# Kernel optimization log

Hardware: AMD Instinct MI355X
Metric: run time of the kernel (lower is better)

## Reference

```python
import jax, jax.numpy as jnp
import numpy as np

FS = 30.0   # sampling_rate from __init__
B, T = 32768, 2048


def setup_inputs() -> dict:
    key = jax.random.key(0)
    x = jax.random.normal(key, (B, T), dtype=jnp.float32)
    return {"x": x}


def _trapz_slice(pairs, a, b):
    # trapz of s[a:b] with dx=1/FS, given precomputed trapezoid pairs
    # pairs[i] = 0.5*(s[i]+s[i+1]); integral sums i in [a, b-2]. Empty slice -> 0.
    i = jnp.arange(pairs.shape[0])
    m = ((i >= a) & (i <= b - 2)).astype(pairs.dtype)
    return jnp.sum(pairs * m) / FS


def _features(s):
    n = s.shape[0]
    # ---- time-domain: [max, ptp, var(ddof=1), std(ddof=1)] ----
    mx = jnp.max(s)
    ptp = mx - jnp.min(s)
    var = jnp.var(s, ddof=1)
    std = jnp.sqrt(var)
    # ---- frequency-domain: mean |FFT| ----
    mean_amp = jnp.mean(jnp.abs(jnp.fft.fft(s)))
    # ---- peak / valley detection on interior points (index i+1 in signal) ----
    l, m_, r = s[:-2], s[1:-1], s[2:]
    peak_m = (l < m_) & (m_ > r)
    val_m = (l > m_) & (m_ < r)
    n_peaks = jnp.sum(peak_m)
    n_vals = jnp.sum(val_m)
    pos = jnp.arange(n - 2)
    p0 = jnp.argmax(peak_m) + 1                       # peaks[0]
    v0 = jnp.argmax(val_m) + 1                        # valleys[0]
    v1 = jnp.argmax(val_m & (pos > (v0 - 1))) + 1     # valleys[1]
    vlast = (n - 3) - jnp.argmax(val_m[::-1]) + 1     # valleys[-1]
    # ---- iPPG features ----
    pairs = 0.5 * (s[:-1] + s[1:])
    PA = _trapz_slice(pairs, v0, vlast)
    A2 = _trapz_slice(pairs, p0, v1)
    PH = s[p0] - s[v0]
    A1 = _trapz_slice(pairs, v0, p0)
    # half-height width between valleys[0] and peaks[0]
    half = 0.5 * (s[p0] + s[v0])
    idx = jnp.arange(n)
    lm = (idx >= v0) & (idx < p0) & (s >= half)
    left_i = jnp.where(jnp.any(lm), jnp.argmax(lm), v0)
    rm = (idx <= p0) & (idx > v0) & (s >= half)
    right_i = jnp.where(jnp.any(rm), (n - 1) - jnp.argmax(rm[::-1]), p0)
    PWHH = (right_i - left_i).astype(s.dtype) / FS
    ippg = jnp.stack([PA, A2, PH, A1, PWHH])
    ippg = jnp.where((n_peaks >= 1) & (n_vals >= 2), ippg, jnp.zeros(5, s.dtype))
    return jnp.concatenate([jnp.stack([mx, ptp, var, std, mean_amp]), ippg])


def reference(x):
    return jax.vmap(_features)(x)  # [B, 10]
```

## Files before the change

kernel.cpp:

```cpp
#include <hip/hip_runtime.h>
#include <math.h>

#define NTH 256

#define CMUL(vr, vi, c, s) { float _tr = (vr)*(c) - (vi)*(s); (vi) = (vr)*(s) + (vi)*(c); (vr) = _tr; }

#define FFT4(r0,i0,r1,i1,r2,i2,r3,i3) {                     \
    float _acr=(r0)+(r2), _aci=(i0)+(i2);                   \
    float _scr=(r0)-(r2), _sci=(i0)-(i2);                   \
    float _bdr=(r1)+(r3), _bdi=(i1)+(i3);                   \
    float _sdr=(r1)-(r3), _sdi=(i1)-(i3);                   \
    (r0)=_acr+_bdr; (i0)=_aci+_bdi;                         \
    (r1)=_scr+_sdi; (i1)=_sci-_sdr;                         \
    (r2)=_acr-_bdr; (i2)=_aci-_bdi;                         \
    (r3)=_scr-_sdi; (i3)=_sci+_sdr; }

__device__ __forceinline__ void fft16(float* xr, float* xi) {
    const float C1 = 0.92387953251128675613f;
    const float S1 = 0.38268343236508977172f;
    const float R2 = 0.70710678118654752440f;
#pragma unroll
    for (int q = 0; q < 4; ++q)
        FFT4(xr[q], xi[q], xr[4+q], xi[4+q], xr[8+q], xi[8+q], xr[12+q], xi[12+q]);
    CMUL(xr[5],  xi[5],   C1, -S1);
    CMUL(xr[9],  xi[9],   R2, -R2);
    CMUL(xr[13], xi[13],  S1, -C1);
    CMUL(xr[6],  xi[6],   R2, -R2);
    { float t = xr[10]; xr[10] = xi[10]; xi[10] = -t; }
    CMUL(xr[14], xi[14], -R2, -R2);
    CMUL(xr[7],  xi[7],   S1, -C1);
    CMUL(xr[11], xi[11], -R2, -R2);
    CMUL(xr[15], xi[15], -C1,  S1);
#pragma unroll
    for (int s = 0; s < 4; ++s)
        FFT4(xr[4*s], xi[4*s], xr[4*s+1], xi[4*s+1], xr[4*s+2], xi[4*s+2], xr[4*s+3], xi[4*s+3]);
}

__global__ __launch_bounds__(NTH, 2)
void feat_kernel(const float* __restrict__ gx, float* __restrict__ gout) {
    const int tid = threadIdx.x;
    const int wv  = tid >> 6;
    const int ln  = tid & 63;
    const int row = blockIdx.x * 4 + wv;
    const float* xrow = gx + (size_t)row * 2048;
    float* orow = gout + (size_t)row * 10;

    __shared__ float ZRs[4][1024], ZIs[4][1024];
    float* Zr = ZRs[wv];
    float* Zi = ZIs[wv];

    const int al  = ln & 3;
    const int k2r = ln >> 2;
    const int b5  = ln >> 5;

    const float4* x4 = (const float4*)xrow;
#pragma unroll
    for (int t = 0; t < 8; ++t) {
        float4 u = x4[ln + 64 * t];
        int c  = 2 * ln + 128 * t;
        int a0 = c ^ (2 * t + b5);
        int a1 = a0 ^ 1;
        Zr[a0] = u.x; Zi[a0] = u.y;
        Zr[a1] = u.z; Zi[a1] = u.w;
    }

    float r[32];
    {
        int base = 16 * ln;
#pragma unroll
        for (int j = 0; j < 16; ++j) {
            int a = base + (j ^ k2r);
            r[2*j]   = Zr[a];
            r[2*j+1] = Zi[a];
        }
    }

    float vmax = r[0], vmin = r[0], vsum = 0.0f, vsq = 0.0f;
#pragma unroll
    for (int e = 0; e < 32; ++e) {
        vmax = fmaxf(vmax, r[e]); vmin = fminf(vmin, r[e]);
        vsum += r[e]; vsq = fmaf(r[e], r[e], vsq);
    }
#pragma unroll
    for (int o = 1; o < 64; o <<= 1) {
        vmax = fmaxf(vmax, __shfl_xor(vmax, o, 64));
        vmin = fminf(vmin, __shfl_xor(vmin, o, 64));
        vsum += __shfl_xor(vsum, o, 64);
        vsq  += __shfl_xor(vsq,  o, 64);
    }
    {
        float mean = vsum * (1.0f / 2048.0f);
        float var = (vsq - vsum * mean) * (1.0f / 2047.0f);
        if (ln == 0) {
            orow[0] = vmax;
            orow[1] = vmax - vmin;
            orow[2] = var;
            orow[3] = sqrtf(var);
        }
    }

    float lN = __shfl_up(r[31], 1, 64);
    unsigned aw = 0, bw = 0;
#pragma unroll
    for (int m = 0; m < 32; ++m) {
        float l = (m == 0) ? lN : r[m - 1];
        float c = r[m];
        aw |= (unsigned)(l < c) << m;
        bw |= (unsigned)(l > c) << m;
    }
    unsigned an = __shfl_down(aw, 1, 64) & 1u;
    unsigned bn = __shfl_down(bw, 1, 64) & 1u;
    unsigned pm = aw & ((bw >> 1) | (bn << 31));
    unsigned vm = bw & ((aw >> 1) | (an << 31));
    if (ln == 0)  { pm &= ~1u; vm &= ~1u; }
    if (ln == 63) { pm &= 0x7FFFFFFFu; vm &= 0x7FFFFFFFu; }

    int pk = __popc(pm) | (__popc(vm) << 12);
    int mp = pm ? 32 * ln + __ffs(pm) - 1 : (1 << 30);
    int mv = vm ? 32 * ln + __ffs(vm) - 1 : (1 << 30);
    int Mv = vm ? 32 * ln + 31 - __clz(vm) : -1;
#pragma unroll
    for (int o = 1; o < 64; o <<= 1) {
        pk += __shfl_xor(pk, o, 64);
        mp = min(mp, __shfl_xor(mp, o, 64));
        mv = min(mv, __shfl_xor(mv, o, 64));
        Mv = max(Mv, __shfl_xor(Mv, o, 64));
    }
    const int n_peaks = pk & 0xFFF, n_vals = pk >> 12, p0 = mp, v0 = mv, vlast = Mv;

    {
        float PA = 0.0f, A2f = 0.0f, PH = 0.0f, A1f = 0.0f, PW = 0.0f;
        if (n_peaks >= 1 && n_vals >= 2) {
            int lo = v0 - 32 * ln;
            unsigned sel = (lo < 0) ? 0xFFFFFFFFu : ((lo >= 31) ? 0u : (0xFFFFFFFFu << (lo + 1)));
            unsigned m2 = vm & sel;
            int mv2 = m2 ? 32 * ln + __ffs(m2) - 1 : (1 << 30);
#pragma unroll
            for (int o = 1; o < 64; o <<= 1) mv2 = min(mv2, __shfl_xor(mv2, o, 64));
            const int v1 = mv2;

            auto sAt = [&](int p) -> float {
                int e = p >> 1;
                int a = e ^ (e >> 6);
                return (p & 1) ? Zi[a] : Zr[a];
            };
            float s_v0  = sAt(v0), s_p0 = sAt(p0);
            float s_pm1 = sAt(p0 - 1), s_v1m1 = sAt(v1 - 1), s_vLm1 = sAt(vlast - 1);
            PH = s_p0 - s_v0;
            float half = 0.5f * (s_p0 + s_v0);

            float S1 = 0.0f, S2 = 0.0f, S3 = 0.0f;
            int li = 1 << 30, ri = -1;
#pragma unroll
            for (int m = 0; m < 32; ++m) {
                int i = 32 * ln + m;
                float si = r[m];
                bool geV0 = (i >= v0), geP0 = (i >= p0);
                if (geV0 && !geP0)  S1 += si;
                if (geP0 && i < v1) S2 += si;
                if (geV0 && i < vlast) S3 += si;
                if (si >= half) {
                    if (geV0 && !geP0)     li = min(li, i);
                    if (i > v0 && i <= p0) ri = max(ri, i);
                }
            }
#pragma unroll
            for (int o = 1; o < 64; o <<= 1) {
                S1 += __shfl_xor(S1, o, 64);
                S2 += __shfl_xor(S2, o, 64);
                S3 += __shfl_xor(S3, o, 64);
                li = min(li, __shfl_xor(li, o, 64));
                ri = max(ri, __shfl_xor(ri, o, 64));
            }
            PA  = (S3 - 0.5f * (s_v0 + s_vLm1)) * (1.0f / 30.0f);
            A2f = (v1 > p0) ? (S2 - 0.5f * (s_p0 + s_v1m1)) * (1.0f / 30.0f) : 0.0f;
            A1f = (p0 > v0) ? (S1 - 0.5f * (s_v0 + s_pm1)) * (1.0f / 30.0f) : 0.0f;
            if (li == (1 << 30)) li = v0;
            if (ri < 0)          ri = p0;
            PW = (float)(ri - li) * (1.0f / 30.0f);
        }
        if (ln == 0) {
            orow[5] = PA;
            orow[6] = A2f;
            orow[7] = PH;
            orow[8] = A1f;
            orow[9] = PW;
        }
    }

    float s0, c0;
    __sincosf((float)ln * (-3.14159265358979323846f / 1024.0f), &s0, &c0);

    float ar[16], ai[16];
#pragma unroll
    for (int n2 = 0; n2 < 16; ++n2) {
        int a = (ln ^ n2) + 64 * n2;
        ar[n2] = Zr[a];
        ai[n2] = Zi[a];
    }
    fft16(ar, ai);
    {
        const float cb = c0 * c0 - s0 * s0;
        const float sb = 2.0f * c0 * s0;
        int wb = 16 * ln;
        Zr[wb + k2r] = ar[0];
        Zi[wb + k2r] = ai[0];
        float cc = cb, ss = sb;
#pragma unroll
        for (int k2 = 1; k2 < 16; ++k2) {
            const int idx = (k2 >> 2) + 4 * (k2 & 3);
            CMUL(ar[idx], ai[idx], cc, ss);
            int a = wb + (k2 ^ k2r);
            Zr[a] = ar[idx];
            Zi[a] = ai[idx];
            float nc = cc * cb - ss * sb;
            ss = cc * sb + ss * cb;
            cc = nc;
        }
    }
    {
        int cbase = 16 * al;
#pragma unroll
        for (int b = 0; b < 16; ++b) {
            int a = cbase + (k2r ^ b) + 64 * b;
            ar[b] = Zr[a];
            ai[b] = Zi[a];
        }
    }
    fft16(ar, ai);
    {
        float cA = (al & 1) ? 0.99518472667219688624f : 1.0f;
        float sA = (al & 1) ? -0.09801714032956060199f : 0.0f;
        float cB = (al & 1) ? 0.95694033573220886494f : 0.98078528040323044913f;
        float sB = (al & 1) ? -0.29028467725446236764f : -0.19509032201612826785f;
        float c1 = (al & 2) ? cB : cA;
        float s1 = (al & 2) ? sB : sA;
        float cc = c1, ss = s1;
#pragma unroll
        for (int j = 1; j < 16; ++j) {
            const int idx = (j >> 2) + 4 * (j & 3);
            CMUL(ar[idx], ai[idx], cc, ss);
            float nc = cc * c1 - ss * s1;
            ss = cc * s1 + ss * c1;
            cc = nc;
        }
    }
    {
        const bool hi = (al & 2) != 0;
        const bool b0 = (al & 1) != 0;
        const int g = ((al & 1) << 1) | (al >> 1);
        int fbase = k2r + 256 * g;
#pragma unroll
        for (int idx = 0; idx < 16; ++idx) {
            int j = (idx >> 2) + 4 * (idx & 3);
            float tr = __shfl_xor(ar[idx], 2, 64);
            float ti = __shfl_xor(ai[idx], 2, 64);
            float vr = hi ? (tr - ar[idx]) : (ar[idx] + tr);
            float vi = hi ? (ti - ai[idx]) : (ai[idx] + ti);
            float sr = __shfl_xor(vr, 1, 64);
            float si = __shfl_xor(vi, 1, 64);
            float Xr, Xi;
            if (!b0) { Xr = hi ? (vr + si) : (vr + sr); Xi = hi ? (vi - sr) : (vi + si); }
            else     { Xr = hi ? (sr - vi) : (sr - vr); Xi = hi ? (si + vr) : (si - vi); }
            Zr[fbase + 16 * j] = Xr;
            Zi[fbase + 16 * j] = Xi;
        }
    }

    float amp = 0.0f;
    {
        float rc = c0, rs = s0;
        const float C16 = 0.98078528040323044913f, S16 = 0.19509032201612826785f;
#pragma unroll
        for (int t = 0; t < 8; ++t) {
            int k = ln + 64 * t;
            int m = (1024 - k) & 1023;
            float zr = Zr[k], zi = Zi[k];
            float mr = Zr[m], mi = Zi[m];
            float Er = 0.5f * (zr + mr), Ei = 0.5f * (zi - mi);
            float Or = 0.5f * (zi + mi), Oi = 0.5f * (mr - zr);
            float Pr = Or * rc - Oi * rs, Pi = Or * rs + Oi * rc;
            float x1r = Er + Pr, x1i = Ei + Pi;
            float x2r = Er - Pr, x2i = Ei - Pi;
            amp += 2.0f * (__builtin_amdgcn_sqrtf(x1r * x1r + x1i * x1i) +
                           __builtin_amdgcn_sqrtf(x2r * x2r + x2i * x2i));
            float nr = rc * C16 + rs * S16;
            rs = rs * C16 - rc * S16;
            rc = nr;
        }
        {
            float zr0 = Zr[0], zi0 = Zi[0];
            float q1 = zr0 + zi0, q2 = zr0 - zi0;
            float corr0 = __builtin_amdgcn_sqrtf(q1 * q1) + __builtin_amdgcn_sqrtf(q2 * q2);
            float zr5 = Zr[512], zi5 = Zi[512];
            float c512 = 2.0f * __builtin_amdgcn_sqrtf(zr5 * zr5 + zi5 * zi5);
            amp += (ln == 0) ? (c512 - corr0) : 0.0f;
        }
    }
#pragma unroll
    for (int o = 1; o < 64; o <<= 1) amp += __shfl_xor(amp, o, 64);

    if (ln == 0) {
        orow[4] = amp * (1.0f / 2048.0f);
    }
}

extern "C" void kernel_launch(void* const* d_in, const int* in_sizes, int n_in,
                              void* d_out, int out_size, void* d_ws, size_t ws_size,
                              hipStream_t stream) {
    (void)d_ws; (void)ws_size; (void)n_in; (void)out_size;
    const float* x = (const float*)d_in[0];
    float* out = (float*)d_out;
    int rows = in_sizes[0] / 2048;
    feat_kernel<<<dim3(rows / 4), dim3(NTH), 0, stream>>>(x, out);
}
```

Measured before the change: 394.9 us.

## Interleave real/imag in shared memory and vectorize FFT math with float2

Replaces the split real/imaginary shared arrays with an interleaved float2 array, so each complex load or store becomes a single 64-bit LDS access instead of two 32-bit ones. The FFT butterflies, twiddle multiplies, statistics and the real-FFT postprocessing are rewritten with 2-wide vector types, which lets the compiler emit packed FP32 instructions. The cost is a possible change in LDS bank-conflict behaviour with 8-byte accesses under the existing XOR swizzles, and possibly more register pressure.

```diff
diff --git a/kernel.cpp b/kernel.cpp
--- a/kernel.cpp
+++ b/kernel.cpp
@@ -3,37 +3,39 @@
 
 #define NTH 256
 
-#define CMUL(vr, vi, c, s) { float _tr = (vr)*(c) - (vi)*(s); (vi) = (vr)*(s) + (vi)*(c); (vr) = _tr; }
-
-#define FFT4(r0,i0,r1,i1,r2,i2,r3,i3) {                     \
-    float _acr=(r0)+(r2), _aci=(i0)+(i2);                   \
-    float _scr=(r0)-(r2), _sci=(i0)-(i2);                   \
-    float _bdr=(r1)+(r3), _bdi=(i1)+(i3);                   \
-    float _sdr=(r1)-(r3), _sdi=(i1)-(i3);                   \
-    (r0)=_acr+_bdr; (i0)=_aci+_bdi;                         \
-    (r1)=_scr+_sdi; (i1)=_sci-_sdr;                         \
-    (r2)=_acr-_bdr; (i2)=_aci-_bdi;                         \
-    (r3)=_scr-_sdi; (i3)=_sci+_sdr; }
-
-__device__ __forceinline__ void fft16(float* xr, float* xi) {
+typedef __attribute__((ext_vector_type(2))) float v2f;
+
+__device__ __forceinline__ v2f cmulv(v2f z, float c, float s) {
+    v2f t; t.x = -z.y; t.y = z.x;
+    return z * c + t * s;
+}
+
+#define FFT4V(z0,z1,z2,z3) {                      \
+    v2f _ac = (z0) + (z2), _sc = (z0) - (z2);     \
+    v2f _bd = (z1) + (z3), _sd = (z1) - (z3);     \
+    v2f _jd; _jd.x = _sd.y; _jd.y = -_sd.x;       \
+    (z0) = _ac + _bd;                             \
+    (z1) = _sc + _jd;                             \
+    (z2) = _ac - _bd;                             \
+    (z3) = _sc - _jd; }
+
+__device__ __forceinline__ void fft16v(v2f* z) {
     const float C1 = 0.92387953251128675613f;
     const float S1 = 0.38268343236508977172f;
     const float R2 = 0.70710678118654752440f;
 #pragma unroll
-    for (int q = 0; q < 4; ++q)
-        FFT4(xr[q], xi[q], xr[4+q], xi[4+q], xr[8+q], xi[8+q], xr[12+q], xi[12+q]);
-    CMUL(xr[5],  xi[5],   C1, -S1);
-    CMUL(xr[9],  xi[9],   R2, -R2);
-    CMUL(xr[13], xi[13],  S1, -C1);
-    CMUL(xr[6],  xi[6],   R2, -R2);
-    { float t = xr[10]; xr[10] = xi[10]; xi[10] = -t; }
-    CMUL(xr[14], xi[14], -R2, -R2);
-    CMUL(xr[7],  xi[7],   S1, -C1);
-    CMUL(xr[11], xi[11], -R2, -R2);
-    CMUL(xr[15], xi[15], -C1,  S1);
-#pragma unroll
-    for (int s = 0; s < 4; ++s)
-        FFT4(xr[4*s], xi[4*s], xr[4*s+1], xi[4*s+1], xr[4*s+2], xi[4*s+2], xr[4*s+3], xi[4*s+3]);
+    for (int q = 0; q < 4; ++q) FFT4V(z[q], z[4+q], z[8+q], z[12+q]);
+    z[5]  = cmulv(z[5],   C1, -S1);
+    z[9]  = cmulv(z[9],   R2, -R2);
+    z[13] = cmulv(z[13],  S1, -C1);
+    z[6]  = cmulv(z[6],   R2, -R2);
+    { v2f t; t.x = z[10].y; t.y = -z[10].x; z[10] = t; }
+    z[14] = cmulv(z[14], -R2, -R2);
+    z[7]  = cmulv(z[7],   S1, -C1);
+    z[11] = cmulv(z[11], -R2, -R2);
+    z[15] = cmulv(z[15], -C1,  S1);
+#pragma unroll
+    for (int s = 0; s < 4; ++s) FFT4V(z[4*s], z[4*s+1], z[4*s+2], z[4*s+3]);
 }
 
 __global__ __launch_bounds__(NTH, 2)
@@ -45,9 +47,8 @@
     const float* xrow = gx + (size_t)row * 2048;
     float* orow = gout + (size_t)row * 10;
 
-    __shared__ float ZRs[4][1024], ZIs[4][1024];
-    float* Zr = ZRs[wv];
-    float* Zi = ZIs[wv];
+    __shared__ v2f Zs_[4][1024];
+    v2f* Zs = Zs_[wv];
 
     const int al  = ln & 3;
     const int k2r = ln >> 2;
@@ -60,27 +61,31 @@
         int c  = 2 * ln + 128 * t;
         int a0 = c ^ (2 * t + b5);
         int a1 = a0 ^ 1;
-        Zr[a0] = u.x; Zi[a0] = u.y;
-        Zr[a1] = u.z; Zi[a1] = u.w;
-    }
-
-    float r[32];
+        v2f w0; w0.x = u.x; w0.y = u.y;
+        v2f w1; w1.x = u.z; w1.y = u.w;
+        Zs[a0] = w0;
+        Zs[a1] = w1;
+    }
+
+    v2f r2[16];
     {
         int base = 16 * ln;
 #pragma unroll
-        for (int j = 0; j < 16; ++j) {
-            int a = base + (j ^ k2r);
-            r[2*j]   = Zr[a];
-            r[2*j+1] = Zi[a];
-        }
-    }
-
-    float vmax = r[0], vmin = r[0], vsum = 0.0f, vsq = 0.0f;
-#pragma unroll
-    for (int e = 0; e < 32; ++e) {
-        vmax = fmaxf(vmax, r[e]); vmin = fminf(vmin, r[e]);
-        vsum += r[e]; vsq = fmaf(r[e], r[e], vsq);
-    }
+        for (int j = 0; j < 16; ++j)
+            r2[j] = Zs[base + (j ^ k2r)];
+    }
+
+    v2f mx2 = r2[0], mn2 = r2[0], sm2 = r2[0], sq2 = r2[0] * r2[0];
+#pragma unroll
+    for (int j = 1; j < 16; ++j) {
+        v2f e = r2[j];
+        mx2.x = fmaxf(mx2.x, e.x); mx2.y = fmaxf(mx2.y, e.y);
+        mn2.x = fminf(mn2.x, e.x); mn2.y = fminf(mn2.y, e.y);
+        sm2 += e;
+        sq2 = e * e + sq2;
+    }
+    float vmax = fmaxf(mx2.x, mx2.y), vmin = fminf(mn2.x, mn2.y);
+    float vsum = sm2.x + sm2.y, vsq = sq2.x + sq2.y;
 #pragma unroll
     for (int o = 1; o < 64; o <<= 1) {
         vmax = fmaxf(vmax, __shfl_xor(vmax, o, 64));
@@ -99,14 +104,16 @@
         }
     }
 
-    float lN = __shfl_up(r[31], 1, 64);
+    float lN = __shfl_up(r2[15].y, 1, 64);
     unsigned aw = 0, bw = 0;
 #pragma unroll
-    for (int m = 0; m < 32; ++m) {
-        float l = (m == 0) ? lN : r[m - 1];
-        float c = r[m];
-        aw |= (unsigned)(l < c) << m;
-        bw |= (unsigned)(l > c) << m;
+    for (int j = 0; j < 16; ++j) {
+        float pv = (j == 0) ? lN : r2[j - 1].y;
+        float e0 = r2[j].x, e1 = r2[j].y;
+        aw |= (unsigned)(pv < e0) << (2 * j);
+        bw |= (unsigned)(pv > e0) << (2 * j);
+        aw |= (unsigned)(e0 < e1) << (2 * j + 1);
+        bw |= (unsigned)(e0 > e1) << (2 * j + 1);
     }
     unsigned an = __shfl_down(aw, 1, 64) & 1u;
     unsigned bn = __shfl_down(bw, 1, 64) & 1u;
@@ -141,8 +148,8 @@
 
             auto sAt = [&](int p) -> float {
                 int e = p >> 1;
-                int a = e ^ (e >> 6);
-                return (p & 1) ? Zi[a] : Zr[a];
+                v2f zz = Zs[e ^ (e >> 6)];
+                return (p & 1) ? zz.y : zz.x;
             };
             float s_v0  = sAt(v0), s_p0 = sAt(p0);
             float s_pm1 = sAt(p0 - 1), s_v1m1 = sAt(v1 - 1), s_vLm1 = sAt(vlast - 1);
@@ -152,16 +159,19 @@
             float S1 = 0.0f, S2 = 0.0f, S3 = 0.0f;
             int li = 1 << 30, ri = -1;
 #pragma unroll
-            for (int m = 0; m < 32; ++m) {
-                int i = 32 * ln + m;
-                float si = r[m];
-                bool geV0 = (i >= v0), geP0 = (i >= p0);
-                if (geV0 && !geP0)  S1 += si;
-                if (geP0 && i < v1) S2 += si;
-                if (geV0 && i < vlast) S3 += si;
-                if (si >= half) {
-                    if (geV0 && !geP0)     li = min(li, i);
-                    if (i > v0 && i <= p0) ri = max(ri, i);
+            for (int j = 0; j < 16; ++j) {
+#pragma unroll
+                for (int h = 0; h < 2; ++h) {
+                    int i = 32 * ln + 2 * j + h;
+                    float si = h ? r2[j].y : r2[j].x;
+                    bool geV0 = (i >= v0), geP0 = (i >= p0);
+                    if (geV0 && !geP0)  S1 += si;
+                    if (geP0 && i < v1) S2 += si;
+                    if (geV0 && i < vlast) S3 += si;
+                    if (si >= half) {
+                        if (geV0 && !geP0)     li = min(li, i);
+                        if (i > v0 && i <= p0) ri = max(ri, i);
+                    }
                 }
             }
 #pragma unroll
@@ -191,43 +201,32 @@
     float s0, c0;
     __sincosf((float)ln * (-3.14159265358979323846f / 1024.0f), &s0, &c0);
 
-    float ar[16], ai[16];
-#pragma unroll
-    for (int n2 = 0; n2 < 16; ++n2) {
-        int a = (ln ^ n2) + 64 * n2;
-        ar[n2] = Zr[a];
-        ai[n2] = Zi[a];
-    }
-    fft16(ar, ai);
+    v2f az[16];
+#pragma unroll
+    for (int n2 = 0; n2 < 16; ++n2)
+        az[n2] = Zs[(ln ^ n2) + 64 * n2];
+    fft16v(az);
     {
         const float cb = c0 * c0 - s0 * s0;
         const float sb = 2.0f * c0 * s0;
         int wb = 16 * ln;
-        Zr[wb + k2r] = ar[0];
-        Zi[wb + k2r] = ai[0];
-        float cc = cb, ss = sb;
+        Zs[wb + k2r] = az[0];
+        v2f w; w.x = cb; w.y = sb;
 #pragma unroll
         for (int k2 = 1; k2 < 16; ++k2) {
             const int idx = (k2 >> 2) + 4 * (k2 & 3);
-            CMUL(ar[idx], ai[idx], cc, ss);
-            int a = wb + (k2 ^ k2r);
-            Zr[a] = ar[idx];
-            Zi[a] = ai[idx];
-            float nc = cc * cb - ss * sb;
-            ss = cc * sb + ss * cb;
-            cc = nc;
+            az[idx] = cmulv(az[idx], w.x, w.y);
+            Zs[wb + (k2 ^ k2r)] = az[idx];
+            w = cmulv(w, cb, sb);
         }
     }
     {
         int cbase = 16 * al;
 #pragma unroll
-        for (int b = 0; b < 16; ++b) {
-            int a = cbase + (k2r ^ b) + 64 * b;
-            ar[b] = Zr[a];
-            ai[b] = Zi[a];
-        }
-    }
-    fft16(ar, ai);
+        for (int b = 0; b < 16; ++b)
+            az[b] = Zs[cbase + (k2r ^ b) + 64 * b];
+    }
+    fft16v(az);
     {
         float cA = (al & 1) ? 0.99518472667219688624f : 1.0f;
         float sA = (al & 1) ? -0.09801714032956060199f : 0.0f;
@@ -235,14 +234,12 @@
         float sB = (al & 1) ? -0.29028467725446236764f : -0.19509032201612826785f;
         float c1 = (al & 2) ? cB : cA;
         float s1 = (al & 2) ? sB : sA;
-        float cc = c1, ss = s1;
+        v2f w; w.x = c1; w.y = s1;
 #pragma unroll
         for (int j = 1; j < 16; ++j) {
             const int idx = (j >> 2) + 4 * (j & 3);
-            CMUL(ar[idx], ai[idx], cc, ss);
-            float nc = cc * c1 - ss * s1;
-            ss = cc * s1 + ss * c1;
-            cc = nc;
+            az[idx] = cmulv(az[idx], w.x, w.y);
+            w = cmulv(w, c1, s1);
         }
     }
     {
@@ -253,47 +250,48 @@
 #pragma unroll
         for (int idx = 0; idx < 16; ++idx) {
             int j = (idx >> 2) + 4 * (idx & 3);
-            float tr = __shfl_xor(ar[idx], 2, 64);
-            float ti = __shfl_xor(ai[idx], 2, 64);
-            float vr = hi ? (tr - ar[idx]) : (ar[idx] + tr);
-            float vi = hi ? (ti - ai[idx]) : (ai[idx] + ti);
+            float arx = az[idx].x, aix = az[idx].y;
+            float tr = __shfl_xor(arx, 2, 64);
+            float ti = __shfl_xor(aix, 2, 64);
+            float vr = hi ? (tr - arx) : (arx + tr);
+            float vi = hi ? (ti - aix) : (aix + ti);
             float sr = __shfl_xor(vr, 1, 64);
             float si = __shfl_xor(vi, 1, 64);
             float Xr, Xi;
             if (!b0) { Xr = hi ? (vr + si) : (vr + sr); Xi = hi ? (vi - sr) : (vi + si); }
             else     { Xr = hi ? (sr - vi) : (sr - vr); Xi = hi ? (si + vr) : (si - vi); }
-            Zr[fbase + 16 * j] = Xr;
-            Zi[fbase + 16 * j] = Xi;
+            v2f X; X.x = Xr; X.y = Xi;
+            Zs[fbase + 16 * j] = X;
         }
     }
 
     float amp = 0.0f;
     {
-        float rc = c0, rs = s0;
+        v2f rw; rw.x = c0; rw.y = s0;
         const float C16 = 0.98078528040323044913f, S16 = 0.19509032201612826785f;
 #pragma unroll
         for (int t = 0; t < 8; ++t) {
             int k = ln + 64 * t;
             int m = (1024 - k) & 1023;
-            float zr = Zr[k], zi = Zi[k];
-            float mr = Zr[m], mi = Zi[m];
-            float Er = 0.5f * (zr + mr), Ei = 0.5f * (zi - mi);
-            float Or = 0.5f * (zi + mi), Oi = 0.5f * (mr - zr);
-            float Pr = Or * rc - Oi * rs, Pi = Or * rs + Oi * rc;
-            float x1r = Er + Pr, x1i = Ei + Pi;
-            float x2r = Er - Pr, x2i = Ei - Pi;
-            amp += 2.0f * (__builtin_amdgcn_sqrtf(x1r * x1r + x1i * x1i) +
-                           __builtin_amdgcn_sqrtf(x2r * x2r + x2i * x2i));
-            float nr = rc * C16 + rs * S16;
-            rs = rs * C16 - rc * S16;
-            rc = nr;
+            v2f z  = Zs[k];
+            v2f mz = Zs[m];
+            v2f cjm; cjm.x = mz.x; cjm.y = -mz.y;
+            v2f E = (z + cjm) * 0.5f;
+            v2f d = cjm - z;
+            v2f O; O.x = -0.5f * d.y; O.y = 0.5f * d.x;
+            v2f P = cmulv(O, rw.x, rw.y);
+            v2f x1 = E + P, x2 = E - P;
+            v2f d1 = x1 * x1, d2 = x2 * x2;
+            amp += 2.0f * (__builtin_amdgcn_sqrtf(d1.x + d1.y) +
+                           __builtin_amdgcn_sqrtf(d2.x + d2.y));
+            rw = cmulv(rw, C16, -S16);
         }
         {
-            float zr0 = Zr[0], zi0 = Zi[0];
-            float q1 = zr0 + zi0, q2 = zr0 - zi0;
+            v2f z0v = Zs[0];
+            float q1 = z0v.x + z0v.y, q2 = z0v.x - z0v.y;
             float corr0 = __builtin_amdgcn_sqrtf(q1 * q1) + __builtin_amdgcn_sqrtf(q2 * q2);
-            float zr5 = Zr[512], zi5 = Zi[512];
-            float c512 = 2.0f * __builtin_amdgcn_sqrtf(zr5 * zr5 + zi5 * zi5);
+            v2f z5 = Zs[512];
+            float c512 = 2.0f * __builtin_amdgcn_sqrtf(z5.x * z5.x + z5.y * z5.y);
             amp += (ln == 0) ? (c512 - corr0) : 0.0f;
         }
     }
```

After: 403.6 us. +2.2%, slower.
